# Optimization experiments

Hardware: AMD Instinct MI355X
Metric: run time of the kernel (lower is better)

## Reference

```python
import jax, jax.numpy as jnp
import numpy as np

UNITS = 256  # LSTM hidden size per source (units=256)

def setup_inputs() -> dict:
    key = jax.random.key(0)
    ks = jax.random.split(key, 7)
    vocab, embed_dim, seq_len, batch, n_cls = 50000, 256, 512, 64, 20
    x = jax.random.randint(ks[0], (batch, seq_len), 0, vocab)
    emb = jax.random.normal(ks[1], (vocab, embed_dim), jnp.float32) * 0.05
    W = jax.random.normal(ks[2], (embed_dim, 4 * UNITS), jnp.float32) * (1.0 / np.sqrt(embed_dim))
    U = jax.random.normal(ks[3], (UNITS, 4 * UNITS), jnp.float32) * (1.0 / np.sqrt(UNITS))
    # keras unit_forget_bias: forget-gate bias = 1, others 0 (gate order i,f,c,o)
    b = jnp.concatenate([jnp.zeros((UNITS,)), jnp.ones((UNITS,)), jnp.zeros((2 * UNITS,))]).astype(jnp.float32)
    Wd = jax.random.normal(ks[4], (UNITS, n_cls), jnp.float32) * (1.0 / np.sqrt(UNITS))
    bd = jnp.zeros((n_cls,), jnp.float32)
    return {"x": x, "emb": emb, "W": W, "U": U, "b": b, "Wd": Wd, "bd": bd}

def reference(x, emb, W, U, b, Wd, bd):
    # Embedding lookup: [B, T] -> [B, T, D]
    e = emb[x]
    B = e.shape[0]
    # Pre-compute input projections for all timesteps (one big GEMM): [B, T, 4H]
    xz = jnp.einsum('btd,dh->bth', e, W) + b
    h0 = jnp.zeros((B, UNITS), e.dtype)
    c0 = jnp.zeros((B, UNITS), e.dtype)

    def step(carry, zt):
        h, c = carry
        z = zt + h @ U  # [B, 4H]
        i, f, g, o = jnp.split(z, 4, axis=-1)
        i = jax.nn.sigmoid(i)
        f = jax.nn.sigmoid(f)
        g = jnp.tanh(g)
        o = jax.nn.sigmoid(o)
        c_new = f * c + i * g
        h_new = o * jnp.tanh(c_new)
        return (h_new, c_new), None

    (h_T, _), _ = jax.lax.scan(step, (h0, c0), jnp.swapaxes(xz, 0, 1))
    logits = h_T @ Wd + bd
    return jax.nn.softmax(logits, axis=-1)
```

## Files before the change

### kernel.cpp

```cpp
#include <hip/hip_runtime.h>
#include <hip/hip_bf16.h>
#include <math.h>


typedef __bf16 bf16_t;
typedef bf16_t bf16x8 __attribute__((ext_vector_type(8)));
typedef bf16_t bf16x4 __attribute__((ext_vector_type(4)));
typedef float  f32x4  __attribute__((ext_vector_type(4)));
typedef unsigned long long u64;

#define T_SZ 512
#define HID 256
#define G4 1024
#define NCLS 20

#define WS_UPACK 0u
#define WS_WPACK (512u * 1024u)
#define WS_HFIN  (1024u * 1024u)
#define WS_EXCH  (1536u * 1024u)
#define WS_XZ    (2u * 1024u * 1024u)

__global__ void pack_weights(const float* __restrict__ W, const float* __restrict__ U,
                             bf16_t* __restrict__ Wp, bf16_t* __restrict__ Up) {
    int tid  = blockIdx.x * blockDim.x + threadIdx.x;
    int j    = tid & 7;
    int lane = (tid >> 3) & 63;
    int ks   = (tid >> 9) & 7;
    int nt   = tid >> 12;
    int row  = ks * 32 + ((lane >> 4) << 3) + j;
    int col  = nt * 16 + (lane & 15);
    Wp[tid] = (bf16_t)W[row * G4 + col];
    Up[tid] = (bf16_t)U[row * G4 + col];
}

__global__ __launch_bounds__(256) void xz_gemm(const int* __restrict__ x,
                                               const float* __restrict__ emb,
                                               const bf16_t* __restrict__ Wp,
                                               const float* __restrict__ bias,
                                               bf16x4* __restrict__ xz2) {
    int nb   = blockIdx.x & 7;
    int t    = blockIdx.x >> 3;
    int w    = threadIdx.x >> 6;
    int lane = threadIdx.x & 63;
    int l15  = lane & 15;
    int quad = lane >> 4;

    int b_row = w * 16 + l15;
    int tok   = x[b_row * T_SZ + t];
    const float* erow = emb + (size_t)tok * 256;

    bf16x8 afrag[8];
#pragma unroll
    for (int ks = 0; ks < 8; ks++) {
        const float4* p = (const float4*)(erow + ks * 32 + quad * 8);
        float4 v0 = p[0], v1 = p[1];
        bf16x8 a;
        a[0] = (bf16_t)v0.x; a[1] = (bf16_t)v0.y; a[2] = (bf16_t)v0.z; a[3] = (bf16_t)v0.w;
        a[4] = (bf16_t)v1.x; a[5] = (bf16_t)v1.y; a[6] = (bf16_t)v1.z; a[7] = (bf16_t)v1.w;
        afrag[ks] = a;
    }

    const bf16x8* Wf = (const bf16x8*)Wp;

#pragma unroll
    for (int nt = 0; nt < 8; nt++) {
        int ntg = nb * 8 + nt;
        float bv = bias[ntg * 16 + l15];
        f32x4 acc = {bv, bv, bv, bv};
        const bf16x8* bp = Wf + (size_t)(ntg * 8) * 64 + lane;
#pragma unroll
        for (int ks = 0; ks < 8; ks++) {
            bf16x8 bfrag = bp[ks * 64];
            acc = __builtin_amdgcn_mfma_f32_16x16x32_bf16(afrag[ks], bfrag, acc, 0, 0, 0);
        }
        bf16x4 hv;
#pragma unroll
        for (int r = 0; r < 4; r++) hv[r] = (bf16_t)acc[r];
        xz2[((size_t)(t * 4 + w) * 64 + ntg) * 64 + lane] = hv;
    }
}

__device__ __forceinline__ float sigmoid_f(float z) {
    return 1.0f / (1.0f + __expf(-z));
}
__device__ __forceinline__ float tanh_f(float z) {
    float e = __expf(2.0f * z);
    return 1.0f - 2.0f / (e + 1.0f);
}
__device__ __forceinline__ unsigned pack2(float a, float b) {
    unsigned short xs = __builtin_bit_cast(unsigned short, (bf16_t)a);
    unsigned short ys = __builtin_bit_cast(unsigned short, (bf16_t)b);
    return (unsigned)xs | ((unsigned)ys << 16);
}
__device__ __forceinline__ bf16_t unpk_lo(unsigned v) {
    return __builtin_bit_cast(bf16_t, (unsigned short)(v & 0xffffu));
}
__device__ __forceinline__ bf16_t unpk_hi(unsigned v) {
    return __builtin_bit_cast(bf16_t, (unsigned short)(v >> 16));
}

__device__ __forceinline__ void mfma_aB(f32x4& d, bf16x8 a, bf16x8 b) {
    asm("v_mfma_f32_16x16x32_bf16 %0, %1, %2, %0" : "+v"(d) : "v"(a), "a"(b));
}

__global__ __launch_bounds__(512, 2) void lstm_pair(const bf16x4* __restrict__ xz2,
                                                    const bf16_t* __restrict__ Up,
                                                    u64* __restrict__ exch,
                                                    float* __restrict__ hfin) {
    if (blockIdx.x & 4) return;
    const int g    = blockIdx.x & 3;
    const int p    = (blockIdx.x >> 3) & 1;
    const int w    = threadIdx.x >> 6;
    const int lane = threadIdx.x & 63;
    const int l15  = lane & 15;
    const int quad = lane >> 4;

    __shared__ __align__(16) bf16_t h_lds[2][16][264];

    const bf16x8* Uf = (const bf16x8*)Up + lane;
    bf16x8 u[4][8];
#pragma unroll
    for (int G = 0; G < 4; G++) {
        int ntg = G * 16 + p * 8 + w;
#pragma unroll
        for (int ks = 0; ks < 8; ks++)
            u[G][ks] = Uf[(ntg * 8 + ks) * 64];
    }
    asm volatile("" : "+a"(u[0][0]), "+a"(u[0][1]), "+a"(u[0][2]), "+a"(u[0][3]),
                      "+a"(u[0][4]), "+a"(u[0][5]), "+a"(u[0][6]), "+a"(u[0][7]));
    asm volatile("" : "+a"(u[1][0]), "+a"(u[1][1]), "+a"(u[1][2]), "+a"(u[1][3]),
                      "+a"(u[1][4]), "+a"(u[1][5]), "+a"(u[1][6]), "+a"(u[1][7]));
    asm volatile("" : "+a"(u[2][0]), "+a"(u[2][1]), "+a"(u[2][2]), "+a"(u[2][3]),
                      "+a"(u[2][4]), "+a"(u[2][5]), "+a"(u[2][6]), "+a"(u[2][7]));
    asm volatile("" : "+a"(u[3][0]), "+a"(u[3][1]), "+a"(u[3][2]), "+a"(u[3][3]),
                      "+a"(u[3][4]), "+a"(u[3][5]), "+a"(u[3][6]), "+a"(u[3][7]));

    for (int i = threadIdx.x; i < 2 * 16 * 264; i += 512)
        (&h_lds[0][0][0])[i] = (bf16_t)0.0f;

    f32x4 cst = {0.f, 0.f, 0.f, 0.f};

    bf16x4 xzv[4];
#pragma unroll
    for (int G = 0; G < 4; G++)
        xzv[G] = xz2[((size_t)(0 * 4 + g) * 64 + (G * 16 + p * 8 + w)) * 64 + lane];

    __syncthreads();

    for (int t = 0; t < T_SZ; t++) {
        const int buf  = t & 1;
        const int nbuf = buf ^ 1;
        const unsigned key = ((unsigned)(t >> 3) + 1u) << 24;

        bf16x8 af[8];
#pragma unroll
        for (int ks = 0; ks < 8; ks++)
            af[ks] = *(const bf16x8*)&h_lds[buf][l15][ks * 32 + quad * 8];

        f32x4 acc[4];
#pragma unroll
        for (int G = 0; G < 4; G++) {
            bf16x4 xv = xzv[G];
            f32x4 a = {(float)xv[0], (float)xv[1], (float)xv[2], (float)xv[3]};
            acc[G] = a;
        }
#pragma unroll
        for (int ks = 0; ks < 8; ks++)
#pragma unroll
            for (int G = 0; G < 4; G++)
                mfma_aB(acc[G], af[ks], u[G][ks]);

        if (t + 1 < T_SZ) {
#pragma unroll
            for (int G = 0; G < 4; G++)
                xzv[G] = xz2[((size_t)((t + 1) * 4 + g) * 64 + (G * 16 + p * 8 + w)) * 64 + lane];
        }

        float hv[4];
#pragma unroll
        for (int r = 0; r < 4; r++) {
            float ig = sigmoid_f(acc[0][r]);
            float fg = sigmoid_f(acc[1][r]);
            float gg = tanh_f(acc[2][r]);
            float og = sigmoid_f(acc[3][r]);
            float cn = fg * cst[r] + ig * gg;
            cst[r] = cn;
            hv[r] = og * tanh_f(cn);
        }

        if (t == T_SZ - 1) {
#pragma unroll
            for (int r = 0; r < 4; r++)
                hfin[(g * 16 + quad * 4 + r) * HID + p * 128 + w * 16 + l15] = hv[r];
            break;
        }

        {
            unsigned dw0 = pack2(hv[0], hv[1]);
            unsigned dw1 = pack2(hv[2], hv[3]);
            u64 q0 = (u64)dw0 | ((u64)(dw0 ^ key) << 32);
            u64 q1 = (u64)dw1 | ((u64)(dw1 ^ key) << 32);
            unsigned base = (((unsigned)(t & 7) * 4 + (unsigned)g) * 2 + (unsigned)p) * 1024u;
            unsigned ui   = (unsigned)(w * 16 + l15) * 8u + (unsigned)(quad * 2);
            __hip_atomic_store(&exch[base + ui],     q0, __ATOMIC_RELAXED, __HIP_MEMORY_SCOPE_AGENT);
            __hip_atomic_store(&exch[base + ui + 1], q1, __ATOMIC_RELAXED, __HIP_MEMORY_SCOPE_AGENT);
        }

#pragma unroll
        for (int r = 0; r < 4; r++)
            h_lds[nbuf][quad * 4 + r][p * 128 + w * 16 + l15] = (bf16_t)hv[r];

        {
            unsigned pbase = (((unsigned)(t & 7) * 4 + (unsigned)g) * 2 + (unsigned)(1 - p)) * 1024u;
            unsigned i0 = (unsigned)threadIdx.x * 2u;
            u64 q0, q1;
            for (;;) {
                q0 = __hip_atomic_load(&exch[pbase + i0],     __ATOMIC_RELAXED, __HIP_MEMORY_SCOPE_AGENT);
                q1 = __hip_atomic_load(&exch[pbase + i0 + 1], __ATOMIC_RELAXED, __HIP_MEMORY_SCOPE_AGENT);
                bool v0 = ((unsigned)(q0 >> 32)) == (((unsigned)q0) ^ key);
                bool v1 = ((unsigned)(q1 >> 32)) == (((unsigned)q1) ^ key);
                if (v0 && v1) break;
            }
            unsigned d0 = (unsigned)q0, d1 = (unsigned)q1;
            int ul  = (int)(i0 >> 3);
            int qq  = (int)((i0 & 7) >> 1);
            int col = (1 - p) * 128 + ul;
            h_lds[nbuf][qq * 4 + 0][col] = unpk_lo(d0);
            h_lds[nbuf][qq * 4 + 1][col] = unpk_hi(d0);
            h_lds[nbuf][qq * 4 + 2][col] = unpk_lo(d1);
            h_lds[nbuf][qq * 4 + 3][col] = unpk_hi(d1);
        }

        __syncthreads();
    }
}

__global__ void head(const float* __restrict__ hfin, const float* __restrict__ Wd,
                     const float* __restrict__ bd, float* __restrict__ out) {
    __shared__ float hrow[HID];
    __shared__ float lg[32];
    __shared__ float ex[32];
    int b = blockIdx.x, tid = threadIdx.x;
    for (int i = tid; i < HID; i += 64) hrow[i] = hfin[b * HID + i];
    __syncthreads();
    if (tid < NCLS) {
        float acc = bd[tid];
        for (int k = 0; k < HID; k++) acc = fmaf(hrow[k], Wd[k * NCLS + tid], acc);
        lg[tid] = acc;
    }
    __syncthreads();
    if (tid < NCLS) {
        float m = -1e30f;
        for (int jj = 0; jj < NCLS; jj++) m = fmaxf(m, lg[jj]);
        ex[tid] = __expf(lg[tid] - m);
    }
    __syncthreads();
    if (tid < NCLS) {
        float sden = 0.0f;
        for (int jj = 0; jj < NCLS; jj++) sden += ex[jj];
        out[b * NCLS + tid] = ex[tid] / sden;
    }
}

extern "C" void kernel_launch(void* const* d_in, const int* in_sizes, int n_in,
                              void* d_out, int out_size, void* d_ws, size_t ws_size,
                              hipStream_t stream) {
    const int*   x    = (const int*)d_in[0];
    const float* emb  = (const float*)d_in[1];
    const float* W    = (const float*)d_in[2];
    const float* U    = (const float*)d_in[3];
    const float* bias = (const float*)d_in[4];
    const float* Wd   = (const float*)d_in[5];
    const float* bd   = (const float*)d_in[6];
    float* out = (float*)d_out;

    char* ws = (char*)d_ws;
    bf16_t* Up   = (bf16_t*)(ws + WS_UPACK);
    bf16_t* Wp   = (bf16_t*)(ws + WS_WPACK);
    float*  hf   = (float*)(ws + WS_HFIN);
    u64*    exch = (u64*)(ws + WS_EXCH);
    bf16x4* xz2  = (bf16x4*)(ws + WS_XZ);

    pack_weights<<<dim3(1024), dim3(256), 0, stream>>>(W, U, Wp, Up);
    xz_gemm<<<dim3(4096), dim3(256), 0, stream>>>(x, emb, Wp, bias, xz2);
    lstm_pair<<<dim3(16), dim3(512), 0, stream>>>(xz2, Up, exch, hf);
    head<<<dim3(64), dim3(64), 0, stream>>>(hf, Wd, bd, out);
}
```

Measured before the change: 1.457 ms.

## Overlap partner h exchange with local-half MFMA in LSTM recurrence

Splits the per-step recurrent GEMM into two K halves. The half fed by this block's own h columns runs first, and meanwhile the partner block's half of h from the previous step is polled from the global exchange buffer. The partner's h is then written into LDS, a barrier follows, and the remaining MFMAs run. This hides the cross-block exchange latency behind compute and moves the polling off the end-of-step critical path. It adds a second barrier per step and a guarded spin with s_sleep, and the guard's bounded break could silently consume stale data if a partner stalls for too long.

```diff
diff --git a/kernel.cpp b/kernel.cpp
--- a/kernel.cpp
+++ b/kernel.cpp
@@ -103,6 +103,14 @@
     asm("v_mfma_f32_16x16x32_bf16 %0, %1, %2, %0" : "+v"(d) : "v"(a), "a"(b));
 }
 
+__device__ __forceinline__ bool valid_q(u64 q, unsigned key) {
+    return ((unsigned)(q >> 32)) == (((unsigned)q) ^ key);
+}
+
+__device__ __forceinline__ void lds_barrier() {
+    asm volatile("s_waitcnt lgkmcnt(0)\n\ts_barrier" ::: "memory");
+}
+
 __global__ __launch_bounds__(512, 2) void lstm_pair(const bf16x4* __restrict__ xz2,
                                                     const bf16_t* __restrict__ Up,
                                                     u64* __restrict__ exch,
@@ -147,15 +155,27 @@
 
     __syncthreads();
 
+    const unsigned i0 = (unsigned)threadIdx.x * 2u;
+
     for (int t = 0; t < T_SZ; t++) {
         const int buf  = t & 1;
         const int nbuf = buf ^ 1;
-        const unsigned key = ((unsigned)(t >> 3) + 1u) << 24;
+
+        const int tp = t - 1;
+        const unsigned pkey  = ((unsigned)(tp >> 3) + 1u) << 24;
+        const unsigned pbase = (((unsigned)(tp & 7) * 4 + (unsigned)g) * 2 + (unsigned)(1 - p)) * 1024u;
+        u64 pq0 = 0, pq1 = 0;
+        if (t > 0) {
+            pq0 = __hip_atomic_load(&exch[pbase + i0],     __ATOMIC_RELAXED, __HIP_MEMORY_SCOPE_AGENT);
+            pq1 = __hip_atomic_load(&exch[pbase + i0 + 1], __ATOMIC_RELAXED, __HIP_MEMORY_SCOPE_AGENT);
+        }
 
         bf16x8 af[8];
 #pragma unroll
-        for (int ks = 0; ks < 8; ks++)
+        for (int k2 = 0; k2 < 4; k2++) {
+            const int ks = p * 4 + k2;
             af[ks] = *(const bf16x8*)&h_lds[buf][l15][ks * 32 + quad * 8];
+        }
 
         f32x4 acc[4];
 #pragma unroll
@@ -165,15 +185,51 @@
             acc[G] = a;
         }
 #pragma unroll
-        for (int ks = 0; ks < 8; ks++)
+        for (int k2 = 0; k2 < 4; k2++) {
+            const int ks = p * 4 + k2;
 #pragma unroll
             for (int G = 0; G < 4; G++)
                 mfma_aB(acc[G], af[ks], u[G][ks]);
-
+        }
+
+        if (t > 0) {
+            if (!(valid_q(pq0, pkey) && valid_q(pq1, pkey))) {
+                int it = 0;
+                unsigned guard = 0;
+                do {
+                    if (++it > 16) __builtin_amdgcn_s_sleep(1);
+                    if (++guard > (1u << 16)) break;
+                    pq0 = __hip_atomic_load(&exch[pbase + i0],     __ATOMIC_RELAXED, __HIP_MEMORY_SCOPE_AGENT);
+                    pq1 = __hip_atomic_load(&exch[pbase + i0 + 1], __ATOMIC_RELAXED, __HIP_MEMORY_SCOPE_AGENT);
+                } while (!(valid_q(pq0, pkey) && valid_q(pq1, pkey)));
+            }
+            const unsigned d0 = (unsigned)pq0, d1 = (unsigned)pq1;
+            const int ul  = (int)(i0 >> 3);
+            const int qq  = (int)((i0 & 7) >> 1);
+            const int col = (1 - p) * 128 + ul;
+            h_lds[buf][qq * 4 + 0][col] = unpk_lo(d0);
+            h_lds[buf][qq * 4 + 1][col] = unpk_hi(d0);
+            h_lds[buf][qq * 4 + 2][col] = unpk_lo(d1);
+            h_lds[buf][qq * 4 + 3][col] = unpk_hi(d1);
+        }
+        lds_barrier();
+
+#pragma unroll
+        for (int k2 = 0; k2 < 4; k2++) {
+            const int ks = (1 - p) * 4 + k2;
+            af[ks] = *(const bf16x8*)&h_lds[buf][l15][ks * 32 + quad * 8];
+        }
         if (t + 1 < T_SZ) {
 #pragma unroll
             for (int G = 0; G < 4; G++)
                 xzv[G] = xz2[((size_t)((t + 1) * 4 + g) * 64 + (G * 16 + p * 8 + w)) * 64 + lane];
+        }
+#pragma unroll
+        for (int k2 = 0; k2 < 4; k2++) {
+            const int ks = (1 - p) * 4 + k2;
+#pragma unroll
+            for (int G = 0; G < 4; G++)
+                mfma_aB(acc[G], af[ks], u[G][ks]);
         }
 
         float hv[4];
@@ -196,42 +252,22 @@
         }
 
         {
+            const unsigned key   = ((unsigned)(t >> 3) + 1u) << 24;
+            const unsigned sbase = (((unsigned)(t & 7) * 4 + (unsigned)g) * 2 + (unsigned)p) * 1024u;
+            const unsigned ui    = (unsigned)(w * 16 + l15) * 8u + (unsigned)(quad * 2);
             unsigned dw0 = pack2(hv[0], hv[1]);
             unsigned dw1 = pack2(hv[2], hv[3]);
             u64 q0 = (u64)dw0 | ((u64)(dw0 ^ key) << 32);
             u64 q1 = (u64)dw1 | ((u64)(dw1 ^ key) << 32);
-            unsigned base = (((unsigned)(t & 7) * 4 + (unsigned)g) * 2 + (unsigned)p) * 1024u;
-            unsigned ui   = (unsigned)(w * 16 + l15) * 8u + (unsigned)(quad * 2);
-            __hip_atomic_store(&exch[base + ui],     q0, __ATOMIC_RELAXED, __HIP_MEMORY_SCOPE_AGENT);
-            __hip_atomic_store(&exch[base + ui + 1], q1, __ATOMIC_RELAXED, __HIP_MEMORY_SCOPE_AGENT);
+            __hip_atomic_store(&exch[sbase + ui],     q0, __ATOMIC_RELAXED, __HIP_MEMORY_SCOPE_AGENT);
+            __hip_atomic_store(&exch[sbase + ui + 1], q1, __ATOMIC_RELAXED, __HIP_MEMORY_SCOPE_AGENT);
         }
 
 #pragma unroll
         for (int r = 0; r < 4; r++)
             h_lds[nbuf][quad * 4 + r][p * 128 + w * 16 + l15] = (bf16_t)hv[r];
 
-        {
-            unsigned pbase = (((unsigned)(t & 7) * 4 + (unsigned)g) * 2 + (unsigned)(1 - p)) * 1024u;
-            unsigned i0 = (unsigned)threadIdx.x * 2u;
-            u64 q0, q1;
-            for (;;) {
-                q0 = __hip_atomic_load(&exch[pbase + i0],     __ATOMIC_RELAXED, __HIP_MEMORY_SCOPE_AGENT);
-                q1 = __hip_atomic_load(&exch[pbase + i0 + 1], __ATOMIC_RELAXED, __HIP_MEMORY_SCOPE_AGENT);
-                bool v0 = ((unsigned)(q0 >> 32)) == (((unsigned)q0) ^ key);
-                bool v1 = ((unsigned)(q1 >> 32)) == (((unsigned)q1) ^ key);
-                if (v0 && v1) break;
-            }
-            unsigned d0 = (unsigned)q0, d1 = (unsigned)q1;
-            int ul  = (int)(i0 >> 3);
-            int qq  = (int)((i0 & 7) >> 1);
-            int col = (1 - p) * 128 + ul;
-            h_lds[nbuf][qq * 4 + 0][col] = unpk_lo(d0);
-            h_lds[nbuf][qq * 4 + 1][col] = unpk_hi(d0);
-            h_lds[nbuf][qq * 4 + 2][col] = unpk_lo(d1);
-            h_lds[nbuf][qq * 4 + 3][col] = unpk_hi(d1);
-        }
-
-        __syncthreads();
+        lds_barrier();
     }
 }
 
```

After: 5.447 ms. 3.74x slower.
